# Optimization experiments

Measured on AMD Instinct MI355X. Metric: run time of the kernel, lower is better.

Reference implementation:

```python
import jax, jax.numpy as jnp
import numpy as np

N_ATOMS = 25000
N_PAIRS = 500000
C = 64        # pp_nodes[-1] == ii_nodes[-1]
PI_N = 32     # pi_nodes[-1]
NB = 8        # n_basis
N_PROPS = 2   # rank//2 + 1 for rank=3


def setup_inputs() -> dict:
    key = jax.random.key(0)
    ks = jax.random.split(key, 16)
    g = lambda k, s, fan: (jax.random.normal(k, s, jnp.float32) / np.float32(np.sqrt(fan)))
    ind_2 = jax.random.randint(ks[0], (N_PAIRS, 2), 0, N_ATOMS, dtype=jnp.int32)
    p1 = jax.random.normal(ks[1], (N_ATOMS, C), jnp.float32)
    p3 = jax.random.normal(ks[2], (N_ATOMS, 3, C), jnp.float32)
    d3 = jax.random.normal(ks[3], (N_PAIRS, 3), jnp.float32)
    basis = jax.random.normal(ks[4], (N_PAIRS, NB), jnp.float32)
    # InvarLayer params
    W_pi = g(ks[5], (2 * C, PI_N * NB), 2 * C)   # PILayer FF (bias, tanh)
    b_pi = jnp.zeros((PI_N * NB,), jnp.float32)
    W_ii = g(ks[6], (PI_N, C * N_PROPS), PI_N)   # ii layer, no bias
    W_pp = g(ks[7], (C * N_PROPS, C), 2 * C)     # pp layer, no bias
    # EquiVarLayer (rank 3) params
    wi_pix = g(ks[8], (C, C), C)
    wj_pix = g(ks[9], (C, C), C)
    W_ppx = g(ks[10], (C, C), C)                 # pp layer: no bias, no activation
    wi_dot = g(ks[11], (C, C), C)
    wj_dot = g(ks[12], (C, C), C)
    # GCBlock final pp layer (bias, tanh)
    W_pp1 = g(ks[13], (2 * C, 2 * C), 2 * C)
    b_pp1 = jnp.zeros((2 * C,), jnp.float32)
    return dict(ind_2=ind_2, p1=p1, p3=p3, d3=d3, basis=basis,
                W_pi=W_pi, b_pi=b_pi, W_ii=W_ii, W_pp=W_pp,
                wi_pix=wi_pix, wj_pix=wj_pix, W_ppx=W_ppx,
                wi_dot=wi_dot, wj_dot=wj_dot, W_pp1=W_pp1, b_pp1=b_pp1)


def reference(ind_2, p1, p3, d3, basis, W_pi, b_pi, W_ii, W_pp,
              wi_pix, wj_pix, W_ppx, wi_dot, wj_dot, W_pp1, b_pp1):
    ii = ind_2[:, 0]
    jj = ind_2[:, 1]
    n_atoms = p1.shape[0]

    # ---- InvarLayer ----
    # PILayer: gather pair endpoints, FF to [P, PI_N*NB], contract with basis
    inter = jnp.concatenate([p1[ii], p1[jj]], axis=-1)         # [P, 2C]
    inter = jnp.tanh(inter @ W_pi + b_pi)                      # [P, PI_N*NB]
    inter = inter.reshape(-1, PI_N, NB)
    i1_pre = jnp.einsum('pcb,pb->pc', inter, basis)            # [P, PI_N]
    # ii FF (no bias)
    i1 = jnp.tanh(i1_pre @ W_ii)                               # [P, 2C]
    # IPLayer: scatter-sum interactions to atoms
    p1_agg = jax.ops.segment_sum(i1, ii, num_segments=n_atoms) # [N, 2C]
    p1_new = jnp.tanh(p1_agg @ W_pp)                           # [N, C]

    i1_0, i1_1 = jnp.split(i1, N_PROPS, axis=-1)               # each [P, C]

    # ---- EquiVarLayer (rank 3) ----
    # weighted PIXLayer: channel-mix gathered endpoint vectors
    ix = (jnp.einsum('pxc,cd->pxd', p3[ii], wi_pix)
          + jnp.einsum('pxc,cd->pxd', p3[jj], wj_pix))         # [P, 3, C]
    # scale(ix, i1) + scale(diff[:, :, None], i1)
    ix = (ix + d3[:, :, None]) * i1_1[:, None, :]              # [P, 3, C]
    p3_agg = jax.ops.segment_sum(ix, ii, num_segments=n_atoms) # [N, 3, C]
    p3_mixed = jnp.einsum('nxc,cd->nxd', p3_agg, W_ppx)        # [N, 3, C]
    # weighted DotLayer: reduce the equivariant axis
    dotted_p3 = jnp.einsum('nxr,nxr->nr',
                           jnp.einsum('nxc,cr->nxr', p3_mixed, wi_dot),
                           jnp.einsum('nxc,cr->nxr', p3_mixed, wj_dot))  # [N, C]

    # ---- GCBlock stitch ----
    p1t1 = jnp.tanh(jnp.concatenate([p1_new, dotted_p3], axis=-1) @ W_pp1 + b_pp1)  # [N, 2C]
    p1_out, s3 = jnp.split(p1t1, N_PROPS, axis=-1)             # each [N, C]
    p3_out = p3_mixed * s3[:, None, :]                         # [N, 3, C]
    return (p1_out, p3_out, dotted_p3, i1, ix)
```

## Files before the change

kernel.cpp:

```cpp
#include <hip/hip_runtime.h>

#define NP 500000
#define NA 25000

typedef float v2f __attribute__((ext_vector_type(2)));

__device__ __forceinline__ float tanh_fast(float x) {
    float e = __expf(2.0f * x);
    return 1.0f - __fdividef(2.0f, e + 1.0f);
}

__device__ __forceinline__ float readlane_f(float v, int lane) {
    int iv = __builtin_bit_cast(int, v);
    int r = __builtin_amdgcn_readlane(iv, lane);
    return __builtin_bit_cast(float, r);
}

__device__ __forceinline__ float dpp8_reduce(float s) {
    int x;
    x = __builtin_amdgcn_update_dpp(0, __builtin_bit_cast(int, s), 0xB1, 0xF, 0xF, true);
    s += __builtin_bit_cast(float, x);
    x = __builtin_amdgcn_update_dpp(0, __builtin_bit_cast(int, s), 0x4E, 0xF, 0xF, true);
    s += __builtin_bit_cast(float, x);
    x = __builtin_amdgcn_update_dpp(0, __builtin_bit_cast(int, s), 0x141, 0xF, 0xF, true);
    s += __builtin_bit_cast(float, x);
    return s;
}

__device__ __forceinline__ unsigned short f2bf(float x) {
    union { float f; unsigned int u; } c; c.f = x;
    unsigned int r = c.u + 0x7FFFu + ((c.u >> 16) & 1u);
    return (unsigned short)(r >> 16);
}
__device__ __forceinline__ float bf2f(unsigned short h) {
    union { unsigned int u; float f; } c; c.u = ((unsigned int)h) << 16;
    return c.f;
}
__device__ __forceinline__ unsigned int pack2bf(float a, float b) {
    return (unsigned int)f2bf(a) | ((unsigned int)f2bf(b) << 16);
}
__device__ __forceinline__ float lo_bf(unsigned int x) { return bf2f((unsigned short)(x & 0xffffu)); }
__device__ __forceinline__ float hi_bf(unsigned int x) { return bf2f((unsigned short)(x >> 16)); }
__device__ __forceinline__ float lo_bf_f(unsigned int x) {
    return __builtin_bit_cast(float, x << 16);
}
__device__ __forceinline__ float hi_bf_f(unsigned int x) {
    return __builtin_bit_cast(float, x & 0xffff0000u);
}
__device__ __forceinline__ v2f w2_bf(unsigned int x) {
    v2f r;
    r.x = lo_bf_f(x);
    r.y = hi_bf_f(x);
    return r;
}

extern "C" __global__ __launch_bounds__(256, 2)
void k0_uv(const float* __restrict__ p1,
           const float* __restrict__ W_pi,
           const float* __restrict__ b_pi,
           float* __restrict__ u,
           unsigned short* __restrict__ vq)
{
    __shared__ float sW[32 * 256];
    __shared__ float sp1[16 * 64];

    const int t = threadIdx.x;
    const int wv = t >> 6;
    const int l = t & 63;
    const int atom0 = blockIdx.x * 16;

    #pragma unroll
    for (int f = 0; f < 4; ++f) {
        int idx = f * 256 + t;
        int at = atom0 + (idx >> 6);
        int atc = at < NA ? at : NA - 1;
        sp1[idx] = p1[(size_t)atc * 64 + (idx & 63)];
    }

    float accu[4][4] = {{0}}, accv[4][4] = {{0}};

    #pragma unroll
    for (int s = 0; s < 4; ++s) {
        __syncthreads();
        {
            const float4* src = (const float4*)(W_pi + s * 32 * 256);
            float4* dst = (float4*)sW;
            #pragma unroll
            for (int f = 0; f < 8; ++f) dst[f * 256 + t] = src[f * 256 + t];
        }
        __syncthreads();
        const int kbase = (s & 1) * 32;
        #pragma unroll 2
        for (int k = 0; k < 32; ++k) {
            float wq[4];
            #pragma unroll
            for (int q = 0; q < 4; ++q) wq[q] = sW[k * 256 + 64 * q + l];
            #pragma unroll
            for (int a = 0; a < 4; ++a) {
                float pv = sp1[(wv * 4 + a) * 64 + kbase + k];
                #pragma unroll
                for (int q = 0; q < 4; ++q) {
                    if (s < 2) accu[a][q] = fmaf(pv, wq[q], accu[a][q]);
                    else       accv[a][q] = fmaf(pv, wq[q], accv[a][q]);
                }
            }
        }
    }

    #pragma unroll
    for (int a = 0; a < 4; ++a) {
        const int at = atom0 + wv * 4 + a;
        if (at < NA) {
            #pragma unroll
            for (int q = 0; q < 4; ++q)
                u[(size_t)at * 256 + 64 * q + l] = accu[a][q] + b_pi[64 * q + l];
            uint2 vv;
            vv.x = pack2bf(accv[a][0], accv[a][1]);
            vv.y = pack2bf(accv[a][2], accv[a][3]);
            *(uint2*)&vq[(size_t)at * 512 + 8 * l] = vv;
        }
    }
}

extern "C" __global__ __launch_bounds__(256, 4)
void k0_q(const float* __restrict__ p3,
          const float* __restrict__ wi_pix,
          const float* __restrict__ wj_pix,
          const int* __restrict__ ind2,
          int* __restrict__ cnt,
          unsigned short* __restrict__ qi_bf,
          unsigned short* __restrict__ vq)
{
    __shared__ float sWi[64 * 64];
    __shared__ float sWj[64 * 64];

    const int t = threadIdx.x;

    {
        int gp = blockIdx.x * 256 + t;
        if (gp < NP) atomicAdd(&cnt[ind2[2 * gp]], 1);
    }

    {
        const float4* si = (const float4*)wi_pix;
        const float4* sj = (const float4*)wj_pix;
        float4* di = (float4*)sWi;
        float4* dj = (float4*)sWj;
        #pragma unroll
        for (int f = 0; f < 4; ++f) { di[f * 256 + t] = si[f * 256 + t]; dj[f * 256 + t] = sj[f * 256 + t]; }
    }
    __syncthreads();

    const int w = t >> 6;
    const int l = t & 63;
    const int atom = blockIdx.x * 4 + w;

    float val0 = p3[((size_t)atom * 3 + 0) * 64 + l];
    float val1 = p3[((size_t)atom * 3 + 1) * 64 + l];
    float val2 = p3[((size_t)atom * 3 + 2) * 64 + l];

    float ai[3] = {0, 0, 0}, aj[3] = {0, 0, 0};
    #pragma unroll 8
    for (int k = 0; k < 64; ++k) {
        float a0 = readlane_f(val0, k);
        float a1 = readlane_f(val1, k);
        float a2 = readlane_f(val2, k);
        float wi = sWi[k * 64 + l];
        float wj = sWj[k * 64 + l];
        ai[0] = fmaf(a0, wi, ai[0]); aj[0] = fmaf(a0, wj, aj[0]);
        ai[1] = fmaf(a1, wi, ai[1]); aj[1] = fmaf(a1, wj, aj[1]);
        ai[2] = fmaf(a2, wi, ai[2]); aj[2] = fmaf(a2, wj, aj[2]);
    }
    uint2 iu, ju;
    iu.x = pack2bf(ai[0], ai[1]); iu.y = pack2bf(ai[2], 0.0f);
    ju.x = pack2bf(aj[0], aj[1]); ju.y = pack2bf(aj[2], 0.0f);
    *(uint2*)&qi_bf[(size_t)atom * 256 + 4 * l] = iu;
    *(uint2*)&vq[(size_t)atom * 512 + 8 * l + 4] = ju;
}

extern "C" __global__ __launch_bounds__(1024)
void csr_scan(const int* __restrict__ cnt, int* __restrict__ rowstart)
{
    __shared__ int ssum[1024];
    const int t = threadIdx.x;
    const int base = t * 25;

    int s = 0;
    #pragma unroll 5
    for (int i = 0; i < 25; ++i) {
        int idx = base + i;
        s += (idx < NA) ? cnt[idx] : 0;
    }
    ssum[t] = s;
    __syncthreads();
    for (int off = 1; off < 1024; off <<= 1) {
        int vv = (t >= off) ? ssum[t - off] : 0;
        __syncthreads();
        ssum[t] += vv;
        __syncthreads();
    }
    int run = (t > 0) ? ssum[t - 1] : 0;
    for (int i = 0; i < 25; ++i) {
        int idx = base + i;
        if (idx <= NA) rowstart[idx] = run;
        run += (idx < NA) ? cnt[idx] : 0;
    }
}

extern "C" __global__ void k_scatter(const int* __restrict__ ind2,
                                     const int* __restrict__ rowstart,
                                     int* __restrict__ cursor,
                                     int2* __restrict__ plist2)
{
    int p = blockIdx.x * 256 + threadIdx.x;
    if (p < NP) {
        int ii = ind2[2 * p];
        int jj = ind2[2 * p + 1];
        int pos = atomicAdd(&cursor[ii], 1);
        plist2[rowstart[ii] + pos] = make_int2(p, jj);
    }
}

extern "C" __global__ __launch_bounds__(256, 4)
void k_pair(const float* __restrict__ d3,
            const float* __restrict__ basis,
            const float* __restrict__ W_ii,
            const float* __restrict__ u,
            const unsigned short* __restrict__ vq,
            const unsigned short* __restrict__ qi_bf,
            const int* __restrict__ rowstart,
            const int2* __restrict__ plist2,
            float* __restrict__ out_i1,
            float* __restrict__ out_ix,
            float* __restrict__ p1_agg,
            float* __restrict__ p3_agg)
{
    const int t = threadIdx.x;
    const int w = t >> 6;
    const int l = t & 63;
    const int n = blockIdx.x * 4 + w;

    unsigned int wAB[32];
    #pragma unroll
    for (int c = 0; c < 32; ++c)
        wAB[c] = pack2bf(W_ii[c * 128 + l], W_ii[c * 128 + 64 + l]);

    float uu[4];
    #pragma unroll
    for (int q = 0; q < 4; ++q) uu[q] = u[(size_t)n * 256 + 64 * q + l];
    float qiv[3];
    {
        uint2 iu = *(const uint2*)&qi_bf[(size_t)n * 256 + 4 * l];
        qiv[0] = lo_bf(iu.x); qiv[1] = hi_bf(iu.x); qiv[2] = lo_bf(iu.y);
    }

    const int start = rowstart[n];
    const int end   = rowstart[n + 1];

    float agg1a = 0.0f, agg1b = 0.0f;
    float agg30 = 0.0f, agg31 = 0.0f, agg32 = 0.0f;

    if (start < end) {
        const int last = end - 1;

        int2 pj0, pj1;
        uint4 vq0, vq1;
        float bs0, bs1;
        float d0x, d0y, d0z, d1x, d1y, d1z;

        {
            int iA = start;
            int iB = (start + 1 <= last) ? start + 1 : last;
            pj0 = plist2[iA];
            pj1 = plist2[iB];
            vq0 = *(const uint4*)&vq[(size_t)pj0.y * 512 + 8 * l];
            vq1 = *(const uint4*)&vq[(size_t)pj1.y * 512 + 8 * l];
            bs0 = basis[(size_t)pj0.x * 8 + (l & 7)];
            bs1 = basis[(size_t)pj1.x * 8 + (l & 7)];
            d0x = d3[3 * (size_t)pj0.x + 0]; d0y = d3[3 * (size_t)pj0.x + 1]; d0z = d3[3 * (size_t)pj0.x + 2];
            d1x = d3[3 * (size_t)pj1.x + 0]; d1y = d3[3 * (size_t)pj1.x + 1]; d1z = d3[3 * (size_t)pj1.x + 2];
        }

        for (int it = start; it < end; it += 2) {
            int iC = (it + 2 <= last) ? it + 2 : last;
            int iD = (it + 3 <= last) ? it + 3 : last;
            int2 pjT0 = plist2[iC];
            int2 pjT1 = plist2[iD];
            uint4 vqT0 = *(const uint4*)&vq[(size_t)pjT0.y * 512 + 8 * l];
            uint4 vqT1 = *(const uint4*)&vq[(size_t)pjT1.y * 512 + 8 * l];
            float bsT0 = basis[(size_t)pjT0.x * 8 + (l & 7)];
            float bsT1 = basis[(size_t)pjT1.x * 8 + (l & 7)];
            float dT0x = d3[3 * (size_t)pjT0.x + 0];
            float dT0y = d3[3 * (size_t)pjT0.x + 1];
            float dT0z = d3[3 * (size_t)pjT0.x + 2];
            float dT1x = d3[3 * (size_t)pjT1.x + 0];
            float dT1y = d3[3 * (size_t)pjT1.x + 1];
            float dT1z = d3[3 * (size_t)pjT1.x + 2];

            float h00 = tanh_fast(uu[0] + lo_bf(vq0.x));
            float h10 = tanh_fast(uu[0] + lo_bf(vq1.x));
            float h01 = tanh_fast(uu[1] + hi_bf(vq0.x));
            float h11 = tanh_fast(uu[1] + hi_bf(vq1.x));
            float h02 = tanh_fast(uu[2] + lo_bf(vq0.y));
            float h12 = tanh_fast(uu[2] + lo_bf(vq1.y));
            float h03 = tanh_fast(uu[3] + hi_bf(vq0.y));
            float h13 = tanh_fast(uu[3] + hi_bf(vq1.y));

            float pre0[4], pre1[4];
            pre0[0] = dpp8_reduce(h00 * bs0);
            pre1[0] = dpp8_reduce(h10 * bs1);
            pre0[1] = dpp8_reduce(h01 * bs0);
            pre1[1] = dpp8_reduce(h11 * bs1);
            pre0[2] = dpp8_reduce(h02 * bs0);
            pre1[2] = dpp8_reduce(h12 * bs1);
            pre0[3] = dpp8_reduce(h03 * bs0);
            pre1[3] = dpp8_reduce(h13 * bs1);

            v2f acc0A = {0.0f, 0.0f}, acc0B = {0.0f, 0.0f};
            v2f acc1A = {0.0f, 0.0f}, acc1B = {0.0f, 0.0f};
            #pragma unroll
            for (int c = 0; c < 32; c += 2) {
                float p00 = readlane_f(pre0[c >> 3], 8 * (c & 7));
                float p10 = readlane_f(pre1[c >> 3], 8 * (c & 7));
                float p01 = readlane_f(pre0[(c + 1) >> 3], 8 * ((c + 1) & 7));
                float p11 = readlane_f(pre1[(c + 1) >> 3], 8 * ((c + 1) & 7));
                v2f w0 = w2_bf(wAB[c]);
                v2f w1 = w2_bf(wAB[c + 1]);
                v2f s00 = {p00, p00}, s10 = {p10, p10};
                v2f s01 = {p01, p01}, s11 = {p11, p11};
                acc0A += s00 * w0;
                acc1A += s10 * w0;
                acc0B += s01 * w1;
                acc1B += s11 * w1;
            }
            const float i10_0 = tanh_fast(acc0A.x + acc0B.x);
            const float i11_0 = tanh_fast(acc0A.y + acc0B.y);
            const float i10_1 = tanh_fast(acc1A.x + acc1B.x);
            const float i11_1 = tanh_fast(acc1A.y + acc1B.y);

            {
                const size_t pA = (size_t)pj0.x;
                __builtin_nontemporal_store(i10_0, &out_i1[pA * 128 + l]);
                __builtin_nontemporal_store(i11_0, &out_i1[pA * 128 + 64 + l]);
                agg1a += i10_0;
                agg1b += i11_0;
                float ix0 = (qiv[0] + lo_bf(vq0.z) + d0x) * i11_0;
                float ix1 = (qiv[1] + hi_bf(vq0.z) + d0y) * i11_0;
                float ix2 = (qiv[2] + lo_bf(vq0.w) + d0z) * i11_0;
                __builtin_nontemporal_store(ix0, &out_ix[(pA * 3 + 0) * 64 + l]);
                __builtin_nontemporal_store(ix1, &out_ix[(pA * 3 + 1) * 64 + l]);
                __builtin_nontemporal_store(ix2, &out_ix[(pA * 3 + 2) * 64 + l]);
                agg30 += ix0; agg31 += ix1; agg32 += ix2;
            }
            if (it + 1 < end) {
                const size_t pA = (size_t)pj1.x;
                __builtin_nontemporal_store(i10_1, &out_i1[pA * 128 + l]);
                __builtin_nontemporal_store(i11_1, &out_i1[pA * 128 + 64 + l]);
                agg1a += i10_1;
                agg1b += i11_1;
                float ix0 = (qiv[0] + lo_bf(vq1.z) + d1x) * i11_1;
                float ix1 = (qiv[1] + hi_bf(vq1.z) + d1y) * i11_1;
                float ix2 = (qiv[2] + lo_bf(vq1.w) + d1z) * i11_1;
                __builtin_nontemporal_store(ix0, &out_ix[(pA * 3 + 0) * 64 + l]);
                __builtin_nontemporal_store(ix1, &out_ix[(pA * 3 + 1) * 64 + l]);
                __builtin_nontemporal_store(ix2, &out_ix[(pA * 3 + 2) * 64 + l]);
                agg30 += ix0; agg31 += ix1; agg32 += ix2;
            }

            pj0 = pjT0; vq0 = vqT0; bs0 = bsT0; d0x = dT0x; d0y = dT0y; d0z = dT0z;
            pj1 = pjT1; vq1 = vqT1; bs1 = bsT1; d1x = dT1x; d1y = dT1y; d1z = dT1z;
        }
    }

    p1_agg[(size_t)n * 128 + l]      = agg1a;
    p1_agg[(size_t)n * 128 + 64 + l] = agg1b;
    p3_agg[(size_t)n * 192 + l]       = agg30;
    p3_agg[(size_t)n * 192 + 64 + l]  = agg31;
    p3_agg[(size_t)n * 192 + 128 + l] = agg32;
}

extern "C" __global__ __launch_bounds__(256, 4)
void k3_atoms(const float* __restrict__ p1_agg,
              const float* __restrict__ p3_agg,
              const float* __restrict__ W_pp,
              const float* __restrict__ W_ppx,
              const float* __restrict__ wi_dot,
              const float* __restrict__ wj_dot,
              const float* __restrict__ W_pp1,
              const float* __restrict__ b_pp1,
              float* __restrict__ out_p1,
              float* __restrict__ out_p3,
              float* __restrict__ out_dot)
{
    __shared__ float s1[4][128];
    __shared__ float s3[4][192];
    __shared__ float sPm[4][192];
    __shared__ float sCat[4][128];

    const int w = threadIdx.x >> 6;
    const int l = threadIdx.x & 63;
    const int n = blockIdx.x * 4 + w;

    s1[w][l]      = p1_agg[(size_t)n * 128 + l];
    s1[w][64 + l] = p1_agg[(size_t)n * 128 + 64 + l];
    #pragma unroll
    for (int x = 0; x < 3; ++x)
        s3[w][x * 64 + l] = p3_agg[(size_t)n * 192 + x * 64 + l];
    __syncthreads();

    float pn = 0.0f;
    #pragma unroll 4
    for (int k = 0; k < 128; ++k)
        pn = fmaf(s1[w][k], W_pp[k * 64 + l], pn);
    pn = tanh_fast(pn);

    float pm[3];
    #pragma unroll
    for (int x = 0; x < 3; ++x) {
        float s = 0.0f;
        #pragma unroll 4
        for (int c = 0; c < 64; ++c)
            s = fmaf(s3[w][x * 64 + c], W_ppx[c * 64 + l], s);
        pm[x] = s;
        sPm[w][x * 64 + l] = s;
    }
    __syncthreads();

    float dot = 0.0f;
    #pragma unroll
    for (int x = 0; x < 3; ++x) {
        float vi = 0.0f, vj = 0.0f;
        #pragma unroll 4
        for (int c = 0; c < 64; ++c) {
            float a = sPm[w][x * 64 + c];
            vi = fmaf(a, wi_dot[c * 64 + l], vi);
            vj = fmaf(a, wj_dot[c * 64 + l], vj);
        }
        dot = fmaf(vi, vj, dot);
    }

    sCat[w][l]      = pn;
    sCat[w][64 + l] = dot;
    __syncthreads();

    float u1 = b_pp1[l];
    float u2 = b_pp1[64 + l];
    #pragma unroll 4
    for (int k = 0; k < 128; ++k) {
        float ck = sCat[w][k];
        u1 = fmaf(ck, W_pp1[k * 128 + l], u1);
        u2 = fmaf(ck, W_pp1[k * 128 + 64 + l], u2);
    }
    float p1o = tanh_fast(u1);
    float s3v = tanh_fast(u2);

    out_p1[(size_t)n * 64 + l]  = p1o;
    out_dot[(size_t)n * 64 + l] = dot;
    #pragma unroll
    for (int x = 0; x < 3; ++x)
        out_p3[((size_t)n * 3 + x) * 64 + l] = pm[x] * s3v;
}

extern "C" void kernel_launch(void* const* d_in, const int* in_sizes, int n_in,
                              void* d_out, int out_size, void* d_ws, size_t ws_size,
                              hipStream_t stream)
{
    const int*   ind2   = (const int*)d_in[0];
    const float* p1     = (const float*)d_in[1];
    const float* p3     = (const float*)d_in[2];
    const float* d3     = (const float*)d_in[3];
    const float* basis  = (const float*)d_in[4];
    const float* W_pi   = (const float*)d_in[5];
    const float* b_pi   = (const float*)d_in[6];
    const float* W_ii   = (const float*)d_in[7];
    const float* W_pp   = (const float*)d_in[8];
    const float* wi_pix = (const float*)d_in[9];
    const float* wj_pix = (const float*)d_in[10];
    const float* W_ppx  = (const float*)d_in[11];
    const float* wi_dot = (const float*)d_in[12];
    const float* wj_dot = (const float*)d_in[13];
    const float* W_pp1  = (const float*)d_in[14];
    const float* b_pp1  = (const float*)d_in[15];

    float* out     = (float*)d_out;
    float* out_p1  = out;
    float* out_p3  = out + 1600000;
    float* out_dot = out + 6400000;
    float* out_i1  = out + 8000000;
    float* out_ix  = out + 72000000;

    float*          u      = (float*)d_ws;
    unsigned short* vq     = (unsigned short*)(u + 6400000);
    unsigned short* qi_bf  = vq + 12800000;
    float*          p1_agg = (float*)(qi_bf + 6400000);
    float*          p3_agg = p1_agg + 3200000;
    int2*           plist2 = (int2*)(p3_agg + 4800000);
    int*            cnt      = (int*)(plist2 + 500000);
    int*            rowstart = cnt + 25000;
    int*            cursor   = rowstart + 25001;

    hipMemsetAsync(cnt, 0, (size_t)75001 * sizeof(int), stream);

    dim3 blk(256);
    k0_uv    <<<dim3(1563), blk, 0, stream>>>(p1, W_pi, b_pi, u, vq);
    k0_q     <<<dim3(6250), blk, 0, stream>>>(p3, wi_pix, wj_pix, ind2, cnt,
                                              qi_bf, vq);
    csr_scan <<<dim3(1), dim3(1024), 0, stream>>>(cnt, rowstart);
    k_scatter<<<dim3(1954), blk, 0, stream>>>(ind2, rowstart, cursor, plist2);
    k_pair   <<<dim3(6250), blk, 0, stream>>>(d3, basis, W_ii, u, vq,
                                              qi_bf, rowstart, plist2,
                                              out_i1, out_ix, p1_agg, p3_agg);
    k3_atoms <<<dim3(6250), blk, 0, stream>>>(p1_agg, p3_agg, W_pp, W_ppx,
                                              wi_dot, wj_dot, W_pp1, b_pp1,
                                              out_p1, out_p3, out_dot);
}
```

Baseline: 583.2 us.

## Remap u/vq lane layout so each lane holds 4 consecutive basis terms

```diff
diff --git a/kernel.cpp b/kernel.cpp
--- a/kernel.cpp
+++ b/kernel.cpp
@@ -16,15 +16,9 @@
     return __builtin_bit_cast(float, r);
 }
 
-__device__ __forceinline__ float dpp8_reduce(float s) {
-    int x;
-    x = __builtin_amdgcn_update_dpp(0, __builtin_bit_cast(int, s), 0xB1, 0xF, 0xF, true);
-    s += __builtin_bit_cast(float, x);
-    x = __builtin_amdgcn_update_dpp(0, __builtin_bit_cast(int, s), 0x4E, 0xF, 0xF, true);
-    s += __builtin_bit_cast(float, x);
-    x = __builtin_amdgcn_update_dpp(0, __builtin_bit_cast(int, s), 0x141, 0xF, 0xF, true);
-    s += __builtin_bit_cast(float, x);
-    return s;
+__device__ __forceinline__ float dpp_xor1_add(float s) {
+    int x = __builtin_amdgcn_update_dpp(0, __builtin_bit_cast(int, s), 0xB1, 0xF, 0xF, true);
+    return s + __builtin_bit_cast(float, x);
 }
 
 __device__ __forceinline__ unsigned short f2bf(float x) {
@@ -92,28 +86,36 @@
         const int kbase = (s & 1) * 32;
         #pragma unroll 2
         for (int k = 0; k < 32; ++k) {
-            float wq[4];
-            #pragma unroll
-            for (int q = 0; q < 4; ++q) wq[q] = sW[k * 256 + 64 * q + l];
+            float4 wq = *(const float4*)&sW[k * 256 + 4 * l];
             #pragma unroll
             for (int a = 0; a < 4; ++a) {
                 float pv = sp1[(wv * 4 + a) * 64 + kbase + k];
-                #pragma unroll
-                for (int q = 0; q < 4; ++q) {
-                    if (s < 2) accu[a][q] = fmaf(pv, wq[q], accu[a][q]);
-                    else       accv[a][q] = fmaf(pv, wq[q], accv[a][q]);
+                if (s < 2) {
+                    accu[a][0] = fmaf(pv, wq.x, accu[a][0]);
+                    accu[a][1] = fmaf(pv, wq.y, accu[a][1]);
+                    accu[a][2] = fmaf(pv, wq.z, accu[a][2]);
+                    accu[a][3] = fmaf(pv, wq.w, accu[a][3]);
+                } else {
+                    accv[a][0] = fmaf(pv, wq.x, accv[a][0]);
+                    accv[a][1] = fmaf(pv, wq.y, accv[a][1]);
+                    accv[a][2] = fmaf(pv, wq.z, accv[a][2]);
+                    accv[a][3] = fmaf(pv, wq.w, accv[a][3]);
                 }
             }
         }
     }
 
+    const float4 bp = *(const float4*)&b_pi[4 * l];
     #pragma unroll
     for (int a = 0; a < 4; ++a) {
         const int at = atom0 + wv * 4 + a;
         if (at < NA) {
-            #pragma unroll
-            for (int q = 0; q < 4; ++q)
-                u[(size_t)at * 256 + 64 * q + l] = accu[a][q] + b_pi[64 * q + l];
+            float4 uo;
+            uo.x = accu[a][0] + bp.x;
+            uo.y = accu[a][1] + bp.y;
+            uo.z = accu[a][2] + bp.z;
+            uo.w = accu[a][3] + bp.w;
+            *(float4*)&u[(size_t)at * 256 + 4 * l] = uo;
             uint2 vv;
             vv.x = pack2bf(accv[a][0], accv[a][1]);
             vv.y = pack2bf(accv[a][2], accv[a][3]);
@@ -239,15 +241,14 @@
     const int w = t >> 6;
     const int l = t & 63;
     const int n = blockIdx.x * 4 + w;
+    const int boff = 4 * (l & 1);
 
     unsigned int wAB[32];
     #pragma unroll
     for (int c = 0; c < 32; ++c)
         wAB[c] = pack2bf(W_ii[c * 128 + l], W_ii[c * 128 + 64 + l]);
 
-    float uu[4];
-    #pragma unroll
-    for (int q = 0; q < 4; ++q) uu[q] = u[(size_t)n * 256 + 64 * q + l];
+    const float4 uu = *(const float4*)&u[(size_t)n * 256 + 4 * l];
     float qiv[3];
     {
         uint2 iu = *(const uint2*)&qi_bf[(size_t)n * 256 + 4 * l];
@@ -265,7 +266,7 @@
 
         int2 pj0, pj1;
         uint4 vq0, vq1;
-        float bs0, bs1;
+        float4 bs0, bs1;
         float d0x, d0y, d0z, d1x, d1y, d1z;
 
         {
@@ -275,8 +276,8 @@
             pj1 = plist2[iB];
             vq0 = *(const uint4*)&vq[(size_t)pj0.y * 512 + 8 * l];
             vq1 = *(const uint4*)&vq[(size_t)pj1.y * 512 + 8 * l];
-            bs0 = basis[(size_t)pj0.x * 8 + (l & 7)];
-            bs1 = basis[(size_t)pj1.x * 8 + (l & 7)];
+            bs0 = *(const float4*)&basis[(size_t)pj0.x * 8 + boff];
+            bs1 = *(const float4*)&basis[(size_t)pj1.x * 8 + boff];
             d0x = d3[3 * (size_t)pj0.x + 0]; d0y = d3[3 * (size_t)pj0.x + 1]; d0z = d3[3 * (size_t)pj0.x + 2];
             d1x = d3[3 * (size_t)pj1.x + 0]; d1y = d3[3 * (size_t)pj1.x + 1]; d1z = d3[3 * (size_t)pj1.x + 2];
         }
@@ -288,8 +289,8 @@
             int2 pjT1 = plist2[iD];
             uint4 vqT0 = *(const uint4*)&vq[(size_t)pjT0.y * 512 + 8 * l];
             uint4 vqT1 = *(const uint4*)&vq[(size_t)pjT1.y * 512 + 8 * l];
-            float bsT0 = basis[(size_t)pjT0.x * 8 + (l & 7)];
-            float bsT1 = basis[(size_t)pjT1.x * 8 + (l & 7)];
+            float4 bsT0 = *(const float4*)&basis[(size_t)pjT0.x * 8 + boff];
+            float4 bsT1 = *(const float4*)&basis[(size_t)pjT1.x * 8 + boff];
             float dT0x = d3[3 * (size_t)pjT0.x + 0];
             float dT0y = d3[3 * (size_t)pjT0.x + 1];
             float dT0z = d3[3 * (size_t)pjT0.x + 2];
@@ -297,33 +298,28 @@
             float dT1y = d3[3 * (size_t)pjT1.x + 1];
             float dT1z = d3[3 * (size_t)pjT1.x + 2];
 
-            float h00 = tanh_fast(uu[0] + lo_bf(vq0.x));
-            float h10 = tanh_fast(uu[0] + lo_bf(vq1.x));
-            float h01 = tanh_fast(uu[1] + hi_bf(vq0.x));
-            float h11 = tanh_fast(uu[1] + hi_bf(vq1.x));
-            float h02 = tanh_fast(uu[2] + lo_bf(vq0.y));
-            float h12 = tanh_fast(uu[2] + lo_bf(vq1.y));
-            float h03 = tanh_fast(uu[3] + hi_bf(vq0.y));
-            float h13 = tanh_fast(uu[3] + hi_bf(vq1.y));
-
-            float pre0[4], pre1[4];
-            pre0[0] = dpp8_reduce(h00 * bs0);
-            pre1[0] = dpp8_reduce(h10 * bs1);
-            pre0[1] = dpp8_reduce(h01 * bs0);
-            pre1[1] = dpp8_reduce(h11 * bs1);
-            pre0[2] = dpp8_reduce(h02 * bs0);
-            pre1[2] = dpp8_reduce(h12 * bs1);
-            pre0[3] = dpp8_reduce(h03 * bs0);
-            pre1[3] = dpp8_reduce(h13 * bs1);
+            float h00 = tanh_fast(uu.x + lo_bf(vq0.x));
+            float h10 = tanh_fast(uu.x + lo_bf(vq1.x));
+            float h01 = tanh_fast(uu.y + hi_bf(vq0.x));
+            float h11 = tanh_fast(uu.y + hi_bf(vq1.x));
+            float h02 = tanh_fast(uu.z + lo_bf(vq0.y));
+            float h12 = tanh_fast(uu.z + lo_bf(vq1.y));
+            float h03 = tanh_fast(uu.w + hi_bf(vq0.y));
+            float h13 = tanh_fast(uu.w + hi_bf(vq1.y));
+
+            float part0 = fmaf(h03, bs0.w, fmaf(h02, bs0.z, fmaf(h01, bs0.y, h00 * bs0.x)));
+            float part1 = fmaf(h13, bs1.w, fmaf(h12, bs1.z, fmaf(h11, bs1.y, h10 * bs1.x)));
+            float pre0 = dpp_xor1_add(part0);
+            float pre1 = dpp_xor1_add(part1);
 
             v2f acc0A = {0.0f, 0.0f}, acc0B = {0.0f, 0.0f};
             v2f acc1A = {0.0f, 0.0f}, acc1B = {0.0f, 0.0f};
             #pragma unroll
             for (int c = 0; c < 32; c += 2) {
-                float p00 = readlane_f(pre0[c >> 3], 8 * (c & 7));
-                float p10 = readlane_f(pre1[c >> 3], 8 * (c & 7));
-                float p01 = readlane_f(pre0[(c + 1) >> 3], 8 * ((c + 1) & 7));
-                float p11 = readlane_f(pre1[(c + 1) >> 3], 8 * ((c + 1) & 7));
+                float p00 = readlane_f(pre0, 2 * c);
+                float p10 = readlane_f(pre1, 2 * c);
+                float p01 = readlane_f(pre0, 2 * c + 2);
+                float p11 = readlane_f(pre1, 2 * c + 2);
                 v2f w0 = w2_bf(wAB[c]);
                 v2f w1 = w2_bf(wAB[c + 1]);
                 v2f s00 = {p00, p00}, s10 = {p10, p10};
```

After: 566.1 us. 2.9% less time.
